# Kernel tuning notes

Measured on AMD Instinct MI355X. Metric: run time of the kernel, lower is better.

The kernel has to match this reference:

```python
import jax, jax.numpy as jnp
import numpy as np
from functools import partial

OBS, LATENT, HID = 32, 256, 1024


def setup_inputs() -> dict:
    key = jax.random.key(0)
    ks = jax.random.split(key, 16)
    s = 0.05  # small init keeps tanh/relu activations in a healthy range
    B, T = 128, 256
    inp = {
        "y": jax.random.normal(ks[0], (B, T, OBS), dtype=jnp.float32),
        "horizon": 512,
        # tanh-RNN cell params (torch nn.RNN layout: W_ih [H,I], W_hh [H,H])
        "W_ih": jax.random.normal(ks[1], (LATENT, OBS), dtype=jnp.float32) * s,
        "W_hh": jax.random.normal(ks[2], (LATENT, LATENT), dtype=jnp.float32) * s,
        "b_ih": jax.random.normal(ks[3], (LATENT,), dtype=jnp.float32) * s,
        "b_hh": jax.random.normal(ks[4], (LATENT,), dtype=jnp.float32) * s,
        # psi: 5-layer MLP latent -> hid -> hid -> hid -> hid -> obs
        "W1": jax.random.normal(ks[5], (HID, LATENT), dtype=jnp.float32) * s,
        "b1": jnp.zeros((HID,), dtype=jnp.float32),
        "W2": jax.random.normal(ks[6], (HID, HID), dtype=jnp.float32) * s,
        "b2": jnp.zeros((HID,), dtype=jnp.float32),
        "W3": jax.random.normal(ks[7], (HID, HID), dtype=jnp.float32) * s,
        "b3": jnp.zeros((HID,), dtype=jnp.float32),
        "W4": jax.random.normal(ks[8], (HID, HID), dtype=jnp.float32) * s,
        "b4": jnp.zeros((HID,), dtype=jnp.float32),
        "W5": jax.random.normal(ks[9], (OBS, HID), dtype=jnp.float32) * s,
        "b5": jnp.zeros((OBS,), dtype=jnp.float32),
    }
    return inp


def _psi(z, W1, b1, W2, b2, W3, b3, W4, b4, W5, b5):
    h = jax.nn.relu(z @ W1.T + b1)
    h = jax.nn.relu(h @ W2.T + b2)
    h = jax.nn.relu(h @ W3.T + b3)
    h = jax.nn.relu(h @ W4.T + b4)
    return h @ W5.T + b5  # (B, OBS)


def reference(y, horizon, W_ih, W_hh, b_ih, b_hh,
              W1, b1, W2, b2, W3, b3, W4, b4, W5, b5):
    B, T, S = y.shape
    psi = partial(_psi, W1=W1, b1=b1, W2=W2, b2=b2, W3=W3, b3=b3,
                  W4=W4, b4=b4, W5=W5, b5=b5)

    def cell(z, inp):
        return jnp.tanh(inp @ W_ih.T + b_ih + z @ W_hh.T + b_hh)

    z0 = jnp.zeros((B, y.shape[2]), dtype=y.dtype) if False else jnp.zeros((B, W_hh.shape[0]), dtype=y.dtype)

    # Phase 1: teacher-forced. y_hat[t] = psi(z_t) BEFORE consuming y[:, t].
    def step_tf(z, y_t):
        yh = psi(z)
        return cell(z, y_t), yh

    z, yh1 = jax.lax.scan(step_tf, z0, jnp.swapaxes(y, 0, 1))  # yh1: (T,B,S)

    def step_ar(z, _):
        yh = psi(z)
        return cell(z, yh), yh

    z, yh2 = jax.lax.scan(step_ar, z, None, length=horizon - T)  # (H-T,B,S)

    y_hat = jnp.concatenate([yh1, yh2], axis=0)  # (H,B,S)
    return jnp.swapaxes(y_hat, 0, 1)  # (B,H,S)
```

## Files before the change

kernel.cpp:

```cpp
#include <hip/hip_runtime.h>
#include <stdint.h>


#define BATCH 128
#define TTF   256
#define HOR   512
#define OBS   32
#define LAT   256
#define HID   1024

#define GROUPS  8
#define MEMBERS 32
#define ARBLOCKS (GROUPS * MEMBERS)
#define ARTHREADS 128

typedef __attribute__((ext_vector_type(8))) short short8;
typedef __attribute__((ext_vector_type(4))) float floatx4;

#define OFF_WB1   ((size_t)0)
#define OFF_WB2   (OFF_WB1 + (size_t)HID*LAT*2)
#define OFF_WB3   (OFF_WB2 + (size_t)HID*HID*2)
#define OFF_WB4   (OFF_WB3 + (size_t)HID*HID*2)
#define OFF_WB5   (OFF_WB4 + (size_t)HID*HID*2)
#define OFF_CB    (OFF_WB5 + (size_t)OBS*HID*2)
#define OFF_WHH2  (OFF_CB + (size_t)LAT*4)
#define OFF_WIH2  (OFF_WHH2 + (size_t)64*256*8)
#define OFF_ZF    (OFF_WIH2 + (size_t)8*256*8)
#define OFF_Z     (OFF_ZF + (size_t)BATCH*LAT*4)
#define OFF_WBC   (OFF_Z + (size_t)BATCH*TTF*LAT*2)
#define OFF_HB    (OFF_WBC + (size_t)LAT*288*2)
#define OFF_CTR   (OFF_HB + (size_t)GROUPS*8*16*HID*2)
#define OFF_END   (OFF_CTR + (size_t)GROUPS*512)

__device__ __forceinline__ uint16_t f2bf(float f) {
    uint32_t u = __float_as_uint(f);
    u += 0x7fffu + ((u >> 16) & 1u);
    return (uint16_t)(u >> 16);
}
__device__ __forceinline__ float bflo(uint32_t u) { return __uint_as_float(u << 16); }
__device__ __forceinline__ float bfhi(uint32_t u) { return __uint_as_float(u & 0xffff0000u); }

__device__ __forceinline__ float fast_tanh(float x) {
    float ax = fabsf(x);
    float e  = __expf(-2.f * ax);
    float r  = (1.f - e) / (1.f + e);
    return copysignf(r, x);
}

__device__ __forceinline__ int hswz(int row, int col) {
    return row * 1024 + ((((col >> 3) ^ (row & 7)) << 3) | (col & 7));
}
__device__ __forceinline__ int zswz(int row, int col) {
    return row * 256 + ((((col >> 3) ^ (row & 7)) << 3) | (col & 7));
}

__device__ __forceinline__ void st16_mall(void* p, floatx4 v) {
    asm volatile("global_store_dwordx4 %0, %1, off sc0 sc1"
                 :: "v"(p), "v"(v) : "memory");
}

typedef const __attribute__((address_space(1))) void* gas_t;
typedef __attribute__((address_space(3))) void* las_t;
__device__ __forceinline__ void gl_lds16(const void* g, void* l) {
    __builtin_amdgcn_global_load_lds((gas_t)g, (las_t)l, 16, 0, 0x11);
}

__device__ __forceinline__ void stage_h(const uint16_t* src, uint16_t* dst,
                                        int w, int L) {
    const char* gp = (const char*)src + w * 16384 + L * 16;
    char* lp = (char*)dst + w * 16384;
    #pragma unroll
    for (int i = 0; i < 16; i++)
        gl_lds16(gp + i * 1024, lp + i * 1024);
}

__global__ void k_cvt(const float* __restrict__ s, uint16_t* __restrict__ d, int n) {
    int i = blockIdx.x * 256 + threadIdx.x;
    if (i < n) d[i] = f2bf(s[i]);
}

__global__ void k_cb(const float* __restrict__ a, const float* __restrict__ b,
                     float* __restrict__ c) {
    int j = threadIdx.x;
    c[j] = a[j] + b[j];
}

__global__ void k_pack(const float* __restrict__ w, uint2* __restrict__ dst, int klen) {
    int k4 = blockIdx.x, j = threadIdx.x;
    int k = k4 * 4;
    uint32_t a = f2bf(w[(size_t)j * klen + k + 0]);
    uint32_t b = f2bf(w[(size_t)j * klen + k + 1]);
    uint32_t c = f2bf(w[(size_t)j * klen + k + 2]);
    uint32_t d = f2bf(w[(size_t)j * klen + k + 3]);
    uint2 r; r.x = a | (b << 16); r.y = c | (d << 16);
    dst[k4 * 256 + j] = r;
}

__global__ void k_packc(const float* __restrict__ whh, const float* __restrict__ wih,
                        uint16_t* __restrict__ wbc) {
    int col = blockIdx.x;
    for (int k = threadIdx.x; k < 288; k += 256) {
        float v = (k < 256) ? whh[(size_t)col * 256 + k] : wih[(size_t)col * 32 + (k - 256)];
        wbc[(size_t)col * 288 + k] = f2bf(v);
    }
}

__global__ __launch_bounds__(256) void k_rnn_tf(
    const float* __restrict__ y, const uint2* __restrict__ whh2,
    const uint2* __restrict__ wih2, const float* __restrict__ cb,
    uint16_t* __restrict__ Zg, float* __restrict__ zfinal)
{
    __shared__ alignas(16) float zl[LAT];
    __shared__ alignas(16) float ys[OBS];
    int j = threadIdx.x, b = blockIdx.x;
    zl[j] = 0.f;
    __syncthreads();
    const float4* z4 = (const float4*)zl;
    const float4* y4 = (const float4*)ys;
    for (int t = 0; t < TTF; t++) {
        if (j < OBS) ys[j] = y[(size_t)b * (TTF * OBS) + t * OBS + j];
        Zg[((size_t)b * TTF + t) * LAT + j] = f2bf(zl[j]);
        __syncthreads();
        float acc = cb[j];
        #pragma unroll 8
        for (int k4 = 0; k4 < 64; k4++) {
            uint2 wv = whh2[k4 * 256 + j];
            float4 zq = z4[k4];
            acc += bflo(wv.x) * zq.x + bfhi(wv.x) * zq.y
                 + bflo(wv.y) * zq.z + bfhi(wv.y) * zq.w;
        }
        #pragma unroll
        for (int k4 = 0; k4 < 8; k4++) {
            uint2 wv = wih2[k4 * 256 + j];
            float4 yq = y4[k4];
            acc += bflo(wv.x) * yq.x + bfhi(wv.x) * yq.y
                 + bflo(wv.y) * yq.z + bfhi(wv.y) * yq.w;
        }
        __syncthreads();
        zl[j] = fast_tanh(acc);
    }
    __syncthreads();
    zfinal[(size_t)b * LAT + j] = zl[j];
}

__global__ __launch_bounds__(512) void k_psi_bulk64(
    const uint16_t* __restrict__ Zg,
    const uint16_t* __restrict__ wb1, const uint16_t* __restrict__ wb2,
    const uint16_t* __restrict__ wb3, const uint16_t* __restrict__ wb4,
    const uint16_t* __restrict__ wb5,
    const float* __restrict__ b1, const float* __restrict__ b2,
    const float* __restrict__ b3, const float* __restrict__ b4,
    const float* __restrict__ b5, float* __restrict__ out)
{
    __shared__ uint16_t hbuf[64 * 1024];
    int tid = threadIdx.x;
    int w = tid >> 6, L = tid & 63, lm = L & 15, q = L >> 4;
    int rb = blockIdx.x * 64;
    int colbase = w * 128;
    floatx4 acc[4][8];
    const floatx4 zero = {0.f, 0.f, 0.f, 0.f};

    #pragma unroll
    for (int rf = 0; rf < 4; rf++)
        #pragma unroll
        for (int nt = 0; nt < 8; nt++) acc[rf][nt] = zero;
    for (int kc = 0; kc < 8; kc++) {
        short8 a[4];
        #pragma unroll
        for (int rf = 0; rf < 4; rf++)
            a[rf] = *(const short8*)(Zg + (size_t)(rb + rf * 16 + lm) * LAT + kc * 32 + q * 8);
        #pragma unroll
        for (int nt = 0; nt < 8; nt++) {
            int n = colbase + nt * 16 + lm;
            short8 bf = *(const short8*)(wb1 + (size_t)n * LAT + kc * 32 + q * 8);
            #pragma unroll
            for (int rf = 0; rf < 4; rf++)
                acc[rf][nt] = __builtin_amdgcn_mfma_f32_16x16x32_bf16(a[rf], bf, acc[rf][nt], 0, 0, 0);
        }
    }
    #pragma unroll
    for (int rf = 0; rf < 4; rf++)
        #pragma unroll
        for (int nt = 0; nt < 8; nt++) {
            int col = colbase + nt * 16 + lm;
            float bias = b1[col];
            #pragma unroll
            for (int i = 0; i < 4; i++) {
                int row = rf * 16 + q * 4 + i;
                hbuf[hswz(row, col)] = f2bf(fmaxf(acc[rf][nt][i] + bias, 0.f));
            }
        }
    __syncthreads();

    const uint16_t* wbs[3] = {wb2, wb3, wb4};
    const float*    bbs[3] = {b2, b3, b4};
    for (int ll = 0; ll < 3; ll++) {
        const uint16_t* wb = wbs[ll];
        const float* bb = bbs[ll];
        #pragma unroll
        for (int rf = 0; rf < 4; rf++)
            #pragma unroll
            for (int nt = 0; nt < 8; nt++) acc[rf][nt] = zero;
        for (int kc = 0; kc < 32; kc++) {
            int g = ((kc * 4 + q) ^ (lm & 7)) << 3;
            short8 a[4];
            #pragma unroll
            for (int rf = 0; rf < 4; rf++)
                a[rf] = *(const short8*)(hbuf + (rf * 16 + lm) * 1024 + g);
            #pragma unroll
            for (int nt = 0; nt < 8; nt++) {
                int n = colbase + nt * 16 + lm;
                short8 bf = *(const short8*)(wb + (size_t)n * HID + kc * 32 + q * 8);
                #pragma unroll
                for (int rf = 0; rf < 4; rf++)
                    acc[rf][nt] = __builtin_amdgcn_mfma_f32_16x16x32_bf16(a[rf], bf, acc[rf][nt], 0, 0, 0);
            }
        }
        __syncthreads();
        #pragma unroll
        for (int rf = 0; rf < 4; rf++)
            #pragma unroll
            for (int nt = 0; nt < 8; nt++) {
                int col = colbase + nt * 16 + lm;
                float bias = bb[col];
                #pragma unroll
                for (int i = 0; i < 4; i++) {
                    int row = rf * 16 + q * 4 + i;
                    hbuf[hswz(row, col)] = f2bf(fmaxf(acc[rf][nt][i] + bias, 0.f));
                }
            }
        __syncthreads();
    }

    {
        int rf5 = w >> 1;
        int nb = (w & 1) * 16;
        floatx4 a5 = zero;
        for (int kc = 0; kc < 32; kc++) {
            int g = ((kc * 4 + q) ^ (lm & 7)) << 3;
            short8 a = *(const short8*)(hbuf + (rf5 * 16 + lm) * 1024 + g);
            short8 bf = *(const short8*)(wb5 + (size_t)(nb + lm) * HID + kc * 32 + q * 8);
            a5 = __builtin_amdgcn_mfma_f32_16x16x32_bf16(a, bf, a5, 0, 0, 0);
        }
        int col = nb + lm;
        float bias = b5[col];
        #pragma unroll
        for (int i = 0; i < 4; i++) {
            int r = rb + rf5 * 16 + q * 4 + i;
            int bb_ = r >> 8, tt = r & 255;
            out[(size_t)bb_ * (HOR * OBS) + tt * OBS + col] = a5[i] + bias;
        }
    }
}

__global__ __launch_bounds__(512) void k_psi_bulk(
    const uint16_t* __restrict__ Zg,
    const uint16_t* __restrict__ wb1, const uint16_t* __restrict__ wb2,
    const uint16_t* __restrict__ wb3, const uint16_t* __restrict__ wb4,
    const uint16_t* __restrict__ wb5,
    const float* __restrict__ b1, const float* __restrict__ b2,
    const float* __restrict__ b3, const float* __restrict__ b4,
    const float* __restrict__ b5, float* __restrict__ out)
{
    __shared__ uint16_t hbuf[32 * 1024];
    int tid = threadIdx.x;
    int w = tid >> 6, L = tid & 63, lm = L & 15, q = L >> 4;
    int rb = blockIdx.x * 32;
    int colbase = w * 128;
    floatx4 acc[2][8];
    const floatx4 zero = {0.f, 0.f, 0.f, 0.f};

    #pragma unroll
    for (int mt = 0; mt < 2; mt++)
        #pragma unroll
        for (int nt = 0; nt < 8; nt++) acc[mt][nt] = zero;
    for (int kc = 0; kc < 8; kc++) {
        short8 a0 = *(const short8*)(Zg + (size_t)(rb + lm) * LAT + kc * 32 + q * 8);
        short8 a1 = *(const short8*)(Zg + (size_t)(rb + 16 + lm) * LAT + kc * 32 + q * 8);
        #pragma unroll
        for (int nt = 0; nt < 8; nt++) {
            int n = colbase + nt * 16 + lm;
            short8 bf = *(const short8*)(wb1 + (size_t)n * LAT + kc * 32 + q * 8);
            acc[0][nt] = __builtin_amdgcn_mfma_f32_16x16x32_bf16(a0, bf, acc[0][nt], 0, 0, 0);
            acc[1][nt] = __builtin_amdgcn_mfma_f32_16x16x32_bf16(a1, bf, acc[1][nt], 0, 0, 0);
        }
    }
    #pragma unroll
    for (int mt = 0; mt < 2; mt++)
        #pragma unroll
        for (int nt = 0; nt < 8; nt++) {
            int col = colbase + nt * 16 + lm;
            float bias = b1[col];
            #pragma unroll
            for (int i = 0; i < 4; i++) {
                int row = mt * 16 + q * 4 + i;
                hbuf[hswz(row, col)] = f2bf(fmaxf(acc[mt][nt][i] + bias, 0.f));
            }
        }
    __syncthreads();

    const uint16_t* wbs[3] = {wb2, wb3, wb4};
    const float*    bbs[3] = {b2, b3, b4};
    for (int ll = 0; ll < 3; ll++) {
        const uint16_t* wb = wbs[ll];
        const float* bb = bbs[ll];
        #pragma unroll
        for (int mt = 0; mt < 2; mt++)
            #pragma unroll
            for (int nt = 0; nt < 8; nt++) acc[mt][nt] = zero;
        for (int kc = 0; kc < 32; kc++) {
            int g = ((kc * 4 + q) ^ (lm & 7)) << 3;
            short8 a0 = *(const short8*)(hbuf + lm * 1024 + g);
            short8 a1 = *(const short8*)(hbuf + (16 + lm) * 1024 + g);
            #pragma unroll
            for (int nt = 0; nt < 8; nt++) {
                int n = colbase + nt * 16 + lm;
                short8 bf = *(const short8*)(wb + (size_t)n * HID + kc * 32 + q * 8);
                acc[0][nt] = __builtin_amdgcn_mfma_f32_16x16x32_bf16(a0, bf, acc[0][nt], 0, 0, 0);
                acc[1][nt] = __builtin_amdgcn_mfma_f32_16x16x32_bf16(a1, bf, acc[1][nt], 0, 0, 0);
            }
        }
        __syncthreads();
        #pragma unroll
        for (int mt = 0; mt < 2; mt++)
            #pragma unroll
            for (int nt = 0; nt < 8; nt++) {
                int col = colbase + nt * 16 + lm;
                float bias = bb[col];
                #pragma unroll
                for (int i = 0; i < 4; i++) {
                    int row = mt * 16 + q * 4 + i;
                    hbuf[hswz(row, col)] = f2bf(fmaxf(acc[mt][nt][i] + bias, 0.f));
                }
            }
        __syncthreads();
    }

    if (w < 4) {
        int mt = w >> 1;
        int nb = (w & 1) * 16;
        floatx4 a5 = zero;
        for (int kc = 0; kc < 32; kc++) {
            int g = ((kc * 4 + q) ^ (lm & 7)) << 3;
            short8 a = *(const short8*)(hbuf + (mt * 16 + lm) * 1024 + g);
            short8 bf = *(const short8*)(wb5 + (size_t)(nb + lm) * HID + kc * 32 + q * 8);
            a5 = __builtin_amdgcn_mfma_f32_16x16x32_bf16(a, bf, a5, 0, 0, 0);
        }
        int col = nb + lm;
        float bias = b5[col];
        #pragma unroll
        for (int i = 0; i < 4; i++) {
            int row = mt * 16 + q * 4 + i;
            int r = rb + row;
            int bb_ = r >> 8, tt = r & 255;
            out[(size_t)bb_ * (HOR * OBS) + tt * OBS + col] = a5[i] + bias;
        }
    }
}

__global__ __launch_bounds__(ARTHREADS) void k_ar2(
    const float* __restrict__ zfinal,
    const uint16_t* __restrict__ wb1, const uint16_t* __restrict__ wb2,
    const uint16_t* __restrict__ wb3, const uint16_t* __restrict__ wb4,
    const uint16_t* __restrict__ wb5, const uint16_t* __restrict__ wbc,
    const float* __restrict__ b1g, const float* __restrict__ b2g,
    const float* __restrict__ b3g, const float* __restrict__ b4g,
    const float* __restrict__ b5g, const float* __restrict__ cb,
    uint16_t* __restrict__ hb_all, unsigned* __restrict__ ctr_all,
    float* __restrict__ out)
{
    __shared__ alignas(16) uint16_t hstg[16 * 1024];
    __shared__ alignas(16) uint16_t zst[2 * 16 * 256];
    __shared__ alignas(16) uint16_t yscr[16 * 32];
    __shared__ alignas(16) uint16_t hsl[16 * 32];

    const int tid = threadIdx.x;
    const int g = blockIdx.x >> 5, m = blockIdx.x & 31;
    const int w = tid >> 6, L = tid & 63, lm = L & 15, q = L >> 4, lm7 = lm & 7;
    const int colbase = m * 32;
    const int cl = w * 16 + lm;
    const int rb = g * 16;
    uint16_t* hb = hb_all + (size_t)g * (8 * 16 * HID);
    unsigned* ctr = ctr_all + g * 128;
    const floatx4 zero = {0.f, 0.f, 0.f, 0.f};

    const float b1v = b1g[colbase + cl];
    const float b2v = b2g[colbase + cl];
    const float b3v = b3g[colbase + cl];
    const float b4v = b4g[colbase + cl];
    const float b5v = b5g[cl];
    float cbv[8];
    #pragma unroll
    for (int ct = 0; ct < 8; ct++) cbv[ct] = cb[w * 128 + ct * 16 + lm];

    for (int idx = tid; idx < 16 * 256; idx += ARTHREADS) {
        int r = idx >> 8, c = idx & 255;
        zst[zswz(r, c)] = f2bf(zfinal[(size_t)(rb + r) * LAT + c]);
    }
    __syncthreads();

    #define HOP_ARRIVE(DST) do {                                             \
        __syncthreads();                                                     \
        if (tid < 64) {                                                      \
            int row_ = tid >> 2, gr_ = tid & 3;                              \
            floatx4 vv_ = *(const floatx4*)((const char*)hsl + tid * 16);    \
            int gsw_ = (m * 4 + gr_) ^ (row_ & 7);                           \
            st16_mall((char*)(DST) + row_ * 2048 + gsw_ * 16, vv_);          \
            asm volatile("s_waitcnt vmcnt(0)" ::: "memory");                 \
            if (tid == 0)                                                    \
                __hip_atomic_fetch_add(ctr, 1u, __ATOMIC_RELAXED,            \
                                       __HIP_MEMORY_SCOPE_AGENT);            \
        }                                                                    \
    } while (0)

    #define HOP_WAIT(TGT) do {                                               \
        if (tid == 0) {                                                      \
            while (__hip_atomic_load(ctr, __ATOMIC_RELAXED,                  \
                                     __HIP_MEMORY_SCOPE_AGENT) < (TGT)) {}   \
        }                                                                    \
        __syncthreads();                                                     \
    } while (0)

    #define CCZ(K0, K1) do {                                                 \
        _Pragma("unroll")                                                    \
        for (int ct = 0; ct < 8; ct++) {                                     \
            const uint16_t* bb2_ = wbc + (size_t)(w * 128 + ct * 16 + lm) * 288 + q * 8; \
            _Pragma("unroll")                                                \
            for (int kc = (K0); kc < (K1); kc++) {                           \
                int gz_ = (kc * 4 + q) ^ lm7;                                \
                short8 a_ = *(const short8*)(zcur + lm * 256 + gz_ * 8);     \
                short8 b_ = *(const short8*)(bb2_ + kc * 32);                \
                cc[ct] = __builtin_amdgcn_mfma_f32_16x16x32_bf16(a_, b_, cc[ct], 0, 0, 0); \
            }                                                                \
        }                                                                    \
    } while (0)

    #define MID_COMPUTE(WB, BV) do {                                         \
        floatx4 acc_ = zero;                                                 \
        const uint16_t* bb_ = WB + (size_t)(colbase + cl) * HID + q * 8;     \
        _Pragma("unroll 8")                                                  \
        for (int kc = 0; kc < 32; kc++) {                                    \
            int gh = (kc * 4 + q) ^ lm7;                                     \
            short8 a_ = *(const short8*)(hstg + lm * 1024 + gh * 8);         \
            short8 b_ = *(const short8*)(bb_ + kc * 32);                     \
            acc_ = __builtin_amdgcn_mfma_f32_16x16x32_bf16(a_, b_, acc_, 0, 0, 0); \
        }                                                                    \
        _Pragma("unroll")                                                    \
        for (int i = 0; i < 4; i++)                                          \
            hsl[(q * 4 + i) * 32 + cl] = f2bf(fmaxf(acc_[i] + (BV), 0.f));   \
    } while (0)

    unsigned tgt = 0;
    #pragma unroll 1
    for (int t = 0; t < HOR - TTF; t++) {
        uint16_t* zcur = zst + (t & 1) * (16 * 256);
        uint16_t* znx  = zst + ((t + 1) & 1) * (16 * 256);
        uint16_t* hp = hb + (t & 1) * (4 * 16 * HID);
        uint16_t* h1 = hp;
        uint16_t* h2 = hp + 16 * HID;
        uint16_t* h3 = hp + 2 * 16 * HID;
        uint16_t* h4 = hp + 3 * 16 * HID;

        floatx4 cc[8];
        #pragma unroll
        for (int ct = 0; ct < 8; ct++) cc[ct] = zero;

        {
            floatx4 acc = zero;
            const uint16_t* bb = wb1 + (size_t)(colbase + cl) * LAT + q * 8;
            #pragma unroll
            for (int kc = 0; kc < 8; kc++) {
                int gz = (kc * 4 + q) ^ lm7;
                short8 a = *(const short8*)(zcur + lm * 256 + gz * 8);
                short8 b = *(const short8*)(bb + kc * 32);
                acc = __builtin_amdgcn_mfma_f32_16x16x32_bf16(a, b, acc, 0, 0, 0);
            }
            #pragma unroll
            for (int i = 0; i < 4; i++)
                hsl[(q * 4 + i) * 32 + cl] = f2bf(fmaxf(acc[i] + b1v, 0.f));
        }
        HOP_ARRIVE(h1); tgt += MEMBERS;
        CCZ(0, 2);
        HOP_WAIT(tgt);
        stage_h(h1, hstg, w, L);
        __syncthreads();

        MID_COMPUTE(wb2, b2v);
        HOP_ARRIVE(h2); tgt += MEMBERS;
        CCZ(2, 4);
        HOP_WAIT(tgt);
        stage_h(h2, hstg, w, L);
        __syncthreads();

        MID_COMPUTE(wb3, b3v);
        HOP_ARRIVE(h3); tgt += MEMBERS;
        CCZ(4, 6);
        HOP_WAIT(tgt);
        stage_h(h3, hstg, w, L);
        __syncthreads();

        MID_COMPUTE(wb4, b4v);
        HOP_ARRIVE(h4); tgt += MEMBERS;
        CCZ(6, 8);
        HOP_WAIT(tgt);
        stage_h(h4, hstg, w, L);
        __syncthreads();

        {
            floatx4 a5 = zero;
            const uint16_t* bb = wb5 + (size_t)cl * HID + q * 8;
            #pragma unroll 8
            for (int kc = 0; kc < 32; kc++) {
                int gh = (kc * 4 + q) ^ lm7;
                short8 a = *(const short8*)(hstg + lm * 1024 + gh * 8);
                short8 b = *(const short8*)(bb + kc * 32);
                a5 = __builtin_amdgcn_mfma_f32_16x16x32_bf16(a, b, a5, 0, 0, 0);
            }
            float vout[4];
            #pragma unroll
            for (int i = 0; i < 4; i++) {
                float v = a5[i] + b5v;
                vout[i] = v;
                yscr[(q * 4 + i) * 32 + cl] = f2bf(v);
            }
            if (m == 0) {
                #pragma unroll
                for (int i = 0; i < 4; i++)
                    out[(size_t)(rb + q * 4 + i) * (HOR * OBS) + (TTF + t) * OBS + cl] = vout[i];
            }
        }
        __syncthreads();
        {
            short8 ay = *(const short8*)(yscr + lm * 32 + q * 8);
            #pragma unroll
            for (int ct = 0; ct < 8; ct++) {
                int ccol = w * 128 + ct * 16 + lm;
                const uint16_t* bb2 = wbc + (size_t)ccol * 288 + q * 8;
                short8 b = *(const short8*)(bb2 + 8 * 32);
                floatx4 v = __builtin_amdgcn_mfma_f32_16x16x32_bf16(ay, b, cc[ct], 0, 0, 0);
                #pragma unroll
                for (int i = 0; i < 4; i++)
                    znx[zswz(q * 4 + i, ccol)] = f2bf(fast_tanh(v[i] + cbv[ct]));
            }
        }
        __syncthreads();
    }
    #undef MID_COMPUTE
    #undef CCZ
    #undef HOP_WAIT
    #undef HOP_ARRIVE
}

extern "C" void kernel_launch(void* const* d_in, const int* in_sizes, int n_in,
                              void* d_out, int out_size, void* d_ws, size_t ws_size,
                              hipStream_t stream) {
    (void)in_sizes; (void)n_in; (void)out_size; (void)ws_size;
    const float* y    = (const float*)d_in[0];
    const float* W_ih = (const float*)d_in[2];
    const float* W_hh = (const float*)d_in[3];
    const float* b_ih = (const float*)d_in[4];
    const float* b_hh = (const float*)d_in[5];
    const float* W1   = (const float*)d_in[6];
    const float* b1   = (const float*)d_in[7];
    const float* W2   = (const float*)d_in[8];
    const float* b2   = (const float*)d_in[9];
    const float* W3   = (const float*)d_in[10];
    const float* b3   = (const float*)d_in[11];
    const float* W4   = (const float*)d_in[12];
    const float* b4   = (const float*)d_in[13];
    const float* W5   = (const float*)d_in[14];
    const float* b5   = (const float*)d_in[15];
    float* out = (float*)d_out;
    char* ws = (char*)d_ws;

    uint16_t* WB1  = (uint16_t*)(ws + OFF_WB1);
    uint16_t* WB2  = (uint16_t*)(ws + OFF_WB2);
    uint16_t* WB3  = (uint16_t*)(ws + OFF_WB3);
    uint16_t* WB4  = (uint16_t*)(ws + OFF_WB4);
    uint16_t* WB5  = (uint16_t*)(ws + OFF_WB5);
    float*    CB   = (float*)(ws + OFF_CB);
    uint2*    WHH2 = (uint2*)(ws + OFF_WHH2);
    uint2*    WIH2 = (uint2*)(ws + OFF_WIH2);
    float*    ZF   = (float*)(ws + OFF_ZF);
    uint16_t* Zbuf = (uint16_t*)(ws + OFF_Z);
    uint16_t* WBC  = (uint16_t*)(ws + OFF_WBC);
    uint16_t* HB   = (uint16_t*)(ws + OFF_HB);
    unsigned* CTR  = (unsigned*)(ws + OFF_CTR);

    k_cvt<<<(HID*LAT + 255) / 256, 256, 0, stream>>>(W1, WB1, HID * LAT);
    k_cvt<<<(HID*HID + 255) / 256, 256, 0, stream>>>(W2, WB2, HID * HID);
    k_cvt<<<(HID*HID + 255) / 256, 256, 0, stream>>>(W3, WB3, HID * HID);
    k_cvt<<<(HID*HID + 255) / 256, 256, 0, stream>>>(W4, WB4, HID * HID);
    k_cvt<<<(OBS*HID + 255) / 256, 256, 0, stream>>>(W5, WB5, OBS * HID);
    k_cb<<<1, 256, 0, stream>>>(b_ih, b_hh, CB);
    k_pack<<<64, 256, 0, stream>>>(W_hh, WHH2, LAT);
    k_pack<<<8, 256, 0, stream>>>(W_ih, WIH2, OBS);
    k_packc<<<256, 256, 0, stream>>>(W_hh, W_ih, WBC);
    hipMemsetAsync(CTR, 0, GROUPS * 512, stream);

    k_rnn_tf<<<BATCH, 256, 0, stream>>>(y, WHH2, WIH2, CB, Zbuf, ZF);

    k_psi_bulk64<<<(BATCH * TTF) / 64, 512, 0, stream>>>(
        Zbuf, WB1, WB2, WB3, WB4, WB5, b1, b2, b3, b4, b5, out);
    hipError_t pe = hipGetLastError();
    if (pe != hipSuccess) {
        k_psi_bulk<<<(BATCH * TTF) / 32, 512, 0, stream>>>(
            Zbuf, WB1, WB2, WB3, WB4, WB5, b1, b2, b3, b4, b5, out);
    }

    void* args[] = {
        (void*)&ZF, (void*)&WB1, (void*)&WB2, (void*)&WB3, (void*)&WB4,
        (void*)&WB5, (void*)&WBC, (void*)&b1, (void*)&b2, (void*)&b3,
        (void*)&b4, (void*)&b5, (void*)&CB, (void*)&HB, (void*)&CTR,
        (void*)&out
    };
    hipError_t ce = hipLaunchCooperativeKernel((const void*)k_ar2,
                                               dim3(ARBLOCKS), dim3(ARTHREADS),
                                               args, 0, stream);
    if (ce != hipSuccess) {
        (void)hipGetLastError();
        k_ar2<<<dim3(ARBLOCKS), dim3(ARTHREADS), 0, stream>>>(
            ZF, WB1, WB2, WB3, WB4, WB5, WBC, b1, b2, b3, b4, b5, CB,
            HB, CTR, out);
    }
}
```

Measured before the change: 6.277 ms.

## Rewrite teacher-forced RNN scan as batched MFMA kernel with split-bf16 state

The scalar per-batch-row RNN kernel (128 blocks x 256 threads, FMA dot products) is replaced by a kernel in which each block handles 16 batch rows and computes W_hh·z and W_ih·y with bf16 MFMA instructions. The hidden state is kept in LDS as hi/lo bf16 pairs to keep close to fp32 accuracy, and is double-buffered with a swizzled layout. This targets the serial scan's latency by using matrix cores per step. The cost is that only 8 blocks of 128 threads run, so most of the GPU sits idle, and weights are re-read from global/L2 every step.

Measured after the change: 9.944 ms. 58.4% more time.

```diff
diff --git a/kernel.cpp b/kernel.cpp
--- a/kernel.cpp
+++ b/kernel.cpp
@@ -37,8 +37,9 @@
     u += 0x7fffu + ((u >> 16) & 1u);
     return (uint16_t)(u >> 16);
 }
-__device__ __forceinline__ float bflo(uint32_t u) { return __uint_as_float(u << 16); }
-__device__ __forceinline__ float bfhi(uint32_t u) { return __uint_as_float(u & 0xffff0000u); }
+__device__ __forceinline__ float bf2f(uint16_t h) {
+    return __uint_as_float((uint32_t)h << 16);
+}
 
 __device__ __forceinline__ float fast_tanh(float x) {
     float ax = fabsf(x);
@@ -85,17 +86,6 @@
     c[j] = a[j] + b[j];
 }
 
-__global__ void k_pack(const float* __restrict__ w, uint2* __restrict__ dst, int klen) {
-    int k4 = blockIdx.x, j = threadIdx.x;
-    int k = k4 * 4;
-    uint32_t a = f2bf(w[(size_t)j * klen + k + 0]);
-    uint32_t b = f2bf(w[(size_t)j * klen + k + 1]);
-    uint32_t c = f2bf(w[(size_t)j * klen + k + 2]);
-    uint32_t d = f2bf(w[(size_t)j * klen + k + 3]);
-    uint2 r; r.x = a | (b << 16); r.y = c | (d << 16);
-    dst[k4 * 256 + j] = r;
-}
-
 __global__ void k_packc(const float* __restrict__ whh, const float* __restrict__ wih,
                         uint16_t* __restrict__ wbc) {
     int col = blockIdx.x;
@@ -105,42 +95,100 @@
     }
 }
 
-__global__ __launch_bounds__(256) void k_rnn_tf(
-    const float* __restrict__ y, const uint2* __restrict__ whh2,
-    const uint2* __restrict__ wih2, const float* __restrict__ cb,
-    uint16_t* __restrict__ Zg, float* __restrict__ zfinal)
+__global__ __launch_bounds__(128) void k_rnn_tf2(
+    const float* __restrict__ y, const uint16_t* __restrict__ wbc,
+    const float* __restrict__ cb, uint16_t* __restrict__ Zg,
+    float* __restrict__ zfinal)
 {
-    __shared__ alignas(16) float zl[LAT];
-    __shared__ alignas(16) float ys[OBS];
-    int j = threadIdx.x, b = blockIdx.x;
-    zl[j] = 0.f;
+    __shared__ alignas(16) uint16_t zhi[2][16 * 256];
+    __shared__ alignas(16) uint16_t zlo[2][16 * 256];
+    __shared__ alignas(16) uint16_t ys[16 * 32];
+    const int tid = threadIdx.x;
+    const int w = tid >> 6, L = tid & 63, lm = L & 15, q = L >> 4, lm7 = lm & 7;
+    const int b0 = blockIdx.x * 16;
+    const int yr = tid >> 3, yc = (tid & 7) * 4;
+    const floatx4 zero = {0.f, 0.f, 0.f, 0.f};
+
+    float cbv[8];
+    #pragma unroll
+    for (int ct = 0; ct < 8; ct++) cbv[ct] = cb[w * 128 + ct * 16 + lm];
+
+    for (int idx = tid; idx < 16 * 256; idx += 128) {
+        zhi[0][idx] = 0; zlo[0][idx] = 0;
+    }
     __syncthreads();
-    const float4* z4 = (const float4*)zl;
-    const float4* y4 = (const float4*)ys;
+
+    #pragma unroll 1
     for (int t = 0; t < TTF; t++) {
-        if (j < OBS) ys[j] = y[(size_t)b * (TTF * OBS) + t * OBS + j];
-        Zg[((size_t)b * TTF + t) * LAT + j] = f2bf(zl[j]);
-        __syncthreads();
-        float acc = cb[j];
-        #pragma unroll 8
-        for (int k4 = 0; k4 < 64; k4++) {
-            uint2 wv = whh2[k4 * 256 + j];
-            float4 zq = z4[k4];
-            acc += bflo(wv.x) * zq.x + bfhi(wv.x) * zq.y
-                 + bflo(wv.y) * zq.z + bfhi(wv.y) * zq.w;
-        }
-        #pragma unroll
-        for (int k4 = 0; k4 < 8; k4++) {
-            uint2 wv = wih2[k4 * 256 + j];
-            float4 yq = y4[k4];
-            acc += bflo(wv.x) * yq.x + bfhi(wv.x) * yq.y
-                 + bflo(wv.y) * yq.z + bfhi(wv.y) * yq.w;
-        }
-        __syncthreads();
-        zl[j] = fast_tanh(acc);
-    }
-    __syncthreads();
-    zfinal[(size_t)b * LAT + j] = zl[j];
+        const int cur = t & 1, nxt = cur ^ 1;
+
+        float4 yv = *(const float4*)(y + (size_t)(b0 + yr) * (TTF * OBS) + t * OBS + yc);
+
+        {
+            const uint16_t* zsrc = zhi[cur] + yr * 256;
+            uint16_t* zdst = Zg + ((size_t)(b0 + yr) * TTF + t) * LAT;
+            #pragma unroll
+            for (int k = 0; k < 4; k++) {
+                int gidx = (tid & 7) * 4 + k;
+                *(short8*)(zdst + gidx * 8) =
+                    *(const short8*)(zsrc + ((gidx ^ (yr & 7)) << 3));
+            }
+        }
+
+        floatx4 acc[8];
+        #pragma unroll
+        for (int ct = 0; ct < 8; ct++) acc[ct] = zero;
+        #pragma unroll 1
+        for (int ct = 0; ct < 8; ct++) {
+            const uint16_t* bbw = wbc + (size_t)(w * 128 + ct * 16 + lm) * 288 + q * 8;
+            #pragma unroll
+            for (int kc = 0; kc < 8; kc++) {
+                int gz = (kc * 4 + q) ^ lm7;
+                short8 a = *(const short8*)(zhi[cur] + lm * 256 + gz * 8);
+                short8 b = *(const short8*)(bbw + kc * 32);
+                acc[ct] = __builtin_amdgcn_mfma_f32_16x16x32_bf16(a, b, acc[ct], 0, 0, 0);
+            }
+            #pragma unroll
+            for (int kc = 0; kc < 8; kc++) {
+                int gz = (kc * 4 + q) ^ lm7;
+                short8 a = *(const short8*)(zlo[cur] + lm * 256 + gz * 8);
+                short8 b = *(const short8*)(bbw + kc * 32);
+                acc[ct] = __builtin_amdgcn_mfma_f32_16x16x32_bf16(a, b, acc[ct], 0, 0, 0);
+            }
+        }
+
+        {
+            uint32_t p0 = (uint32_t)f2bf(yv.x) | ((uint32_t)f2bf(yv.y) << 16);
+            uint32_t p1 = (uint32_t)f2bf(yv.z) | ((uint32_t)f2bf(yv.w) << 16);
+            uint2 pk; pk.x = p0; pk.y = p1;
+            *(uint2*)(ys + yr * 32 + yc) = pk;
+        }
+        __syncthreads();
+
+        #pragma unroll 1
+        for (int ct = 0; ct < 8; ct++) {
+            int ccol = w * 128 + ct * 16 + lm;
+            const uint16_t* bbw = wbc + (size_t)ccol * 288 + q * 8;
+            short8 ay = *(const short8*)(ys + lm * 32 + q * 8);
+            short8 b = *(const short8*)(bbw + 8 * 32);
+            floatx4 v = __builtin_amdgcn_mfma_f32_16x16x32_bf16(ay, b, acc[ct], 0, 0, 0);
+            #pragma unroll
+            for (int i = 0; i < 4; i++) {
+                float zv = fast_tanh(v[i] + cbv[ct]);
+                uint16_t h = f2bf(zv);
+                int o = zswz(q * 4 + i, ccol);
+                zhi[nxt][o] = h;
+                zlo[nxt][o] = f2bf(zv - bf2f(h));
+            }
+        }
+        __syncthreads();
+    }
+
+    for (int idx = tid; idx < 16 * 256; idx += 128) {
+        int r = idx >> 8, c = idx & 255;
+        int o = zswz(r, c);
+        zfinal[(size_t)(b0 + r) * LAT + c] = bf2f(zhi[0][o]) + bf2f(zlo[0][o]);
+    }
 }
 
 __global__ __launch_bounds__(512) void k_psi_bulk64(
@@ -579,8 +627,6 @@
     uint16_t* WB4  = (uint16_t*)(ws + OFF_WB4);
     uint16_t* WB5  = (uint16_t*)(ws + OFF_WB5);
     float*    CB   = (float*)(ws + OFF_CB);
-    uint2*    WHH2 = (uint2*)(ws + OFF_WHH2);
-    uint2*    WIH2 = (uint2*)(ws + OFF_WIH2);
     float*    ZF   = (float*)(ws + OFF_ZF);
     uint16_t* Zbuf = (uint16_t*)(ws + OFF_Z);
     uint16_t* WBC  = (uint16_t*)(ws + OFF_WBC);
@@ -593,12 +639,10 @@
     k_cvt<<<(HID*HID + 255) / 256, 256, 0, stream>>>(W4, WB4, HID * HID);
     k_cvt<<<(OBS*HID + 255) / 256, 256, 0, stream>>>(W5, WB5, OBS * HID);
     k_cb<<<1, 256, 0, stream>>>(b_ih, b_hh, CB);
-    k_pack<<<64, 256, 0, stream>>>(W_hh, WHH2, LAT);
-    k_pack<<<8, 256, 0, stream>>>(W_ih, WIH2, OBS);
     k_packc<<<256, 256, 0, stream>>>(W_hh, W_ih, WBC);
     hipMemsetAsync(CTR, 0, GROUPS * 512, stream);
 
-    k_rnn_tf<<<BATCH, 256, 0, stream>>>(y, WHH2, WIH2, CB, Zbuf, ZF);
+    k_rnn_tf2<<<GROUPS, 128, 0, stream>>>(y, WBC, CB, Zbuf, ZF);
 
     k_psi_bulk64<<<(BATCH * TTF) / 64, 512, 0, stream>>>(
         Zbuf, WB1, WB2, WB3, WB4, WB5, b1, b2, b3, b4, b5, out);
```
